# Performance work log

Measured on AMD Instinct MI355X. Metric: run time of the kernel, lower is better.

The kernel has to match this reference:

```python
import jax, jax.numpy as jnp
import numpy as np

B, T, D, H, QK, V, M = 2, 2048, 1024, 16, 64, 64, 1024
SOFTCAP = 50.0


def apply_rope(x, positions, max_wavelength=10000.0):
    # x: (B, T, H, d), positions: (T,)
    d = x.shape[-1]
    fraction = 2.0 * jnp.arange(d // 2, dtype=jnp.float32) / d
    timescale = max_wavelength ** fraction                      # (d/2,)
    sinusoid = positions.astype(jnp.float32)[:, None] / timescale  # (T, d/2)
    sin = jnp.sin(sinusoid)[:, None, :]  # (T, 1, d/2) broadcasts over heads
    cos = jnp.cos(sinusoid)[:, None, :]
    x1, x2 = jnp.split(x, 2, axis=-1)
    out = jnp.concatenate([x1 * cos - x2 * sin, x2 * cos + x1 * sin], axis=-1)
    return out.astype(x.dtype)


def rms_norm(x, scale, eps=1e-6):
    var = jnp.mean(jnp.square(x.astype(jnp.float32)), axis=-1, keepdims=True)
    normed = x * jax.lax.rsqrt(var + eps).astype(x.dtype)
    return normed * (1.0 + scale).astype(x.dtype)


def setup_inputs() -> dict:
    key = jax.random.key(0)
    ks = jax.random.split(key, 10)
    s = 0.02
    # key-padding mask: per-batch kv valid lengths (all rows have >=1536 valid keys)
    kv_lens = jnp.array([1536, 2048], dtype=jnp.int32)
    mask = (jnp.arange(T)[None, :] < kv_lens[:, None])  # (B, Tk)
    mask = jnp.broadcast_to(mask[:, None, None, :], (B, 1, T, T))
    return {
        "q": jax.random.normal(ks[0], (B, T, D), jnp.float32),
        "kv": jax.random.normal(ks[1], (B, T, D), jnp.float32),
        "mask": mask,
        "q_positions": jnp.arange(T, dtype=jnp.int32),
        "kv_positions": jnp.arange(T, dtype=jnp.int32),
        "wq": jax.random.normal(ks[2], (D, H * QK), jnp.float32) * s,
        "bq": jnp.zeros((H * QK,), jnp.float32),
        "wk": jax.random.normal(ks[3], (D, H * QK), jnp.float32) * s,
        "bk": jnp.zeros((H * QK,), jnp.float32),
        "wv": jax.random.normal(ks[4], (D, H * V), jnp.float32) * s,
        "bv": jnp.zeros((H * V,), jnp.float32),
        "q_scale": jnp.zeros((QK,), jnp.float32),
        "k_scale": jnp.zeros((QK,), jnp.float32),
        "wo": jax.random.normal(ks[5], (H * V, M), jnp.float32) * s,
        "bo": jnp.zeros((M,), jnp.float32),
    }


def reference(q, kv, mask, q_positions, kv_positions,
              wq, bq, wk, bk, wv, bv, q_scale, k_scale, wo, bo):
    qh = (q @ wq + bq).reshape(B, T, H, QK)
    kh = (kv @ wk + bk).reshape(B, T, H, QK)
    vh = (kv @ wv + bv).reshape(B, T, H, V)
    # QK RMSNorm
    qh = rms_norm(qh, q_scale)
    kh = rms_norm(kh, k_scale)
    # RoPE
    qh = apply_rope(qh, q_positions)
    kh = apply_rope(kh, kv_positions)
    # softcapped, masked attention
    logits = jnp.einsum("bthd,bThd->bhtT", qh, kh) / np.sqrt(QK).astype(jnp.float32)
    logits = SOFTCAP * jnp.tanh(logits / SOFTCAP)
    logits = jnp.where(mask, logits, -1e9)
    log_probs = jax.nn.log_softmax(logits, axis=-1)
    probs = jnp.exp(log_probs)
    probs = jnp.where(mask, probs, 0.0)
    # normalized attention entropy (B, H, T)
    entropy = -jnp.sum(probs * log_probs, axis=-1) / jnp.log(mask.sum(axis=-1))
    attn = jnp.einsum("bhtT,bThd->bthd", probs, vh).reshape(B, T, H * V)
    out = attn @ wo + bo
    return out, entropy
```

## Files before the change

### kernel.cpp

```cpp
#include <hip/hip_runtime.h>

#define BB 2
#define TT 2048
#define DD 1024
#define HH 16
#define QKD 64
#define VD 64
#define MD 1024

typedef _Float16 half4 __attribute__((ext_vector_type(4)));
typedef _Float16 half8 __attribute__((ext_vector_type(8)));
typedef __fp16 fp16x2 __attribute__((ext_vector_type(2)));
typedef float f32x4 __attribute__((ext_vector_type(4)));
typedef unsigned short us8 __attribute__((ext_vector_type(8)));
typedef unsigned short us4 __attribute__((ext_vector_type(4)));

__device__ __forceinline__ unsigned short f2h(float x){
    union { _Float16 h; unsigned short u; } c; c.h = (_Float16)x; return c.u;
}

__device__ __forceinline__ void gl16(const void* g, void* l){
    __builtin_amdgcn_global_load_lds(
        (const __attribute__((address_space(1))) void*)g,
        (__attribute__((address_space(3))) void*)l, 16, 0, 0);
}

__global__ __launch_bounds__(256) void k_prep(const float* __restrict__ q,
                                              const float* __restrict__ kv,
                                              unsigned short* __restrict__ q_bf,
                                              unsigned short* __restrict__ kv_bf,
                                              const float* __restrict__ w0,
                                              const float* __restrict__ w1,
                                              const float* __restrict__ w2,
                                              const float* __restrict__ w3,
                                              unsigned short* __restrict__ o0,
                                              unsigned short* __restrict__ o1,
                                              unsigned short* __restrict__ o2,
                                              unsigned short* __restrict__ o3,
                                              const int* __restrict__ qpos,
                                              const int* __restrict__ kpos,
                                              float* __restrict__ tabq,
                                              float* __restrict__ tabk,
                                              const unsigned char* __restrict__ mask,
                                              int* __restrict__ kvlen){
    __shared__ float smem[64*65];
    int bid = blockIdx.x, tid = threadIdx.x;
    if (bid < 8192){
        const int n = BB*TT*DD/4;
        int idx = bid*256 + tid;
        const float* src = (idx < n) ? q : kv;
        unsigned short* dst = (idx < n) ? q_bf : kv_bf;
        int i = ((idx < n) ? idx : idx - n)*4;
        const float4 v = *(const float4*)(src + i);
        us4 o; o.x = f2h(v.x); o.y = f2h(v.y); o.z = f2h(v.z); o.w = f2h(v.w);
        *(us4*)(dst + i) = o;
    } else if (bid < 9216){
        int idx2 = bid - 8192;
        int z = idx2 >> 8;
        int rc2 = idx2 & 255;
        const float* in = (z==0) ? w0 : (z==1) ? w1 : (z==2) ? w2 : w3;
        unsigned short* out = (z==0) ? o0 : (z==1) ? o1 : (z==2) ? o2 : o3;
        float (*ts)[65] = (float(*)[65])smem;
        int r0 = (rc2 & 15)*64, c0 = (rc2 >> 4)*64;
        int lr = tid >> 4, lc = (tid & 15)*4;
#pragma unroll
        for (int i = 0; i < 4; ++i){
            const float4 v = *(const float4*)(in + (long)(r0 + lr + i*16)*1024 + c0 + lc);
            ts[lr+i*16][lc+0] = v.x; ts[lr+i*16][lc+1] = v.y;
            ts[lr+i*16][lc+2] = v.z; ts[lr+i*16][lc+3] = v.w;
        }
        __syncthreads();
        int oc = tid >> 2, rc = (tid & 3)*16;
        int ocp = oc;
        if (z < 2){
            int blk = oc >> 4;
            ocp = (blk == 1) ? oc + 16 : ((blk == 2) ? oc - 16 : oc);
        }
        us8 o0v, o1v;
#pragma unroll
        for (int j = 0; j < 8; ++j){ o0v[j] = f2h(ts[rc+j][ocp]); o1v[j] = f2h(ts[rc+8+j][ocp]); }
        *(us8*)(out + (long)(c0+oc)*1024 + r0 + rc)     = o0v;
        *(us8*)(out + (long)(c0+oc)*1024 + r0 + rc + 8) = o1v;
    } else if (bid < 9728){
        int gi = (bid - 9216)*256 + tid;
        const int* pos = (gi < 65536) ? qpos : kpos;
        float* tab = (gi < 65536) ? tabq : tabk;
        int idx = gi & 65535;
        int t = idx >> 5, f = idx & 31;
        float invts = expf(-((float)f*(1.f/32.f)) * 9.210340371976184f);
        float ph = (float)pos[t]*invts;
        ((float2*)tab)[idx] = make_float2(sinf(ph), cosf(ph));
    } else {
        int* red = (int*)smem;
        int b = bid - 9728;
        bool bytemode = (mask[1] != 0);
        int cnt = 0;
        for (int j = tid; j < TT; j += 256){
            long e = (long)b*TT*TT + j;
            if (bytemode) cnt += (mask[e] != 0);
            else          cnt += (((const unsigned int*)mask)[e] != 0);
        }
        red[tid] = cnt; __syncthreads();
        for (int s = 128; s > 0; s >>= 1){ if (tid < s) red[tid] += red[tid+s]; __syncthreads(); }
        if (tid == 0) kvlen[b] = red[0];
    }
}

#define GEMM_CORE(A_, Bt_, abase, bbase)                                            \
    int srow = l >> 3;                                                              \
    int scol = ((l & 7) ^ srow)*8;                                                  \
    int swb = lg ^ (li & 7);                                                        \
    const unsigned short* ga[4]; const unsigned short* gb[2];                       \
    _Pragma("unroll")                                                               \
    for (int i = 0; i < 4; ++i) ga[i] = A_  + (long)(m0 + w*32 + i*8 + srow)*1024 + scol; \
    _Pragma("unroll")                                                               \
    for (int i = 0; i < 2; ++i) gb[i] = Bt_ + (long)(n0 + w*16 + i*8 + srow)*1024 + scol; \
    _Pragma("unroll")                                                               \
    for (int i = 0; i < 4; ++i) gl16(ga[i], abase + (w*32 + i*8)*128);              \
    _Pragma("unroll")                                                               \
    for (int i = 0; i < 2; ++i) gl16(gb[i], bbase + (w*16 + i*8)*128);              \
    __syncthreads();                                                                \
    for (int ks = 0; ks < 16; ++ks){                                                \
        int cur = ks & 1;                                                           \
        if (ks + 1 < 16){                                                           \
            char* an = abase + (cur^1)*16384;                                       \
            char* bn = bbase + (cur^1)*8192;                                        \
            _Pragma("unroll")                                                       \
            for (int i = 0; i < 4; ++i){ ga[i] += 64; gl16(ga[i], an + (w*32 + i*8)*128); } \
            _Pragma("unroll")                                                       \
            for (int i = 0; i < 2; ++i){ gb[i] += 64; gl16(gb[i], bn + (w*16 + i*8)*128); } \
        }                                                                           \
        const char* ac = abase + cur*16384;                                         \
        const char* bc = bbase + cur*8192;                                          \
        _Pragma("unroll")                                                           \
        for (int kk = 0; kk < 2; ++kk){                                             \
            int co = ((kk*4) ^ swb)*16;                                             \
            half8 af[4], bf[2];                                                     \
            _Pragma("unroll")                                                       \
            for (int mi = 0; mi < 4; ++mi) af[mi] = *(const half8*)(ac + (wm + mi*16 + li)*128 + co); \
            _Pragma("unroll")                                                       \
            for (int ni = 0; ni < 2; ++ni) bf[ni] = *(const half8*)(bc + (wn + ni*16 + li)*128 + co); \
            _Pragma("unroll")                                                       \
            for (int mi = 0; mi < 4; ++mi)                                          \
                _Pragma("unroll")                                                   \
                for (int ni = 0; ni < 2; ++ni)                                      \
                    acc[mi][ni] = __builtin_amdgcn_mfma_f32_16x16x32_f16(af[mi], bf[ni], acc[mi][ni], 0, 0, 0); \
        }                                                                           \
        __syncthreads();                                                            \
    }

__global__ __launch_bounds__(256) void k_gemm3(const unsigned short* __restrict__ q_bf,
                                               const unsigned short* __restrict__ kv_bf,
                                               const unsigned short* __restrict__ wqt,
                                               const unsigned short* __restrict__ wkt,
                                               const unsigned short* __restrict__ wvt,
                                               const float* __restrict__ bq,
                                               const float* __restrict__ bk,
                                               const float* __restrict__ bv,
                                               const float* __restrict__ qscale,
                                               const float* __restrict__ kscale,
                                               const float* __restrict__ tabq,
                                               const float* __restrict__ tabk,
                                               unsigned short* __restrict__ Qr,
                                               unsigned short* __restrict__ Kr,
                                               unsigned short* __restrict__ VTb){
    __shared__ float4 smem_[3072];
    char* abase = (char*)smem_;
    char* bbase = abase + 32768;
    int flat = blockIdx.x;
    int virt = (flat & 7)*192 + (flat >> 3);
    int z = virt >> 9;
    int rem = virt & 511;
    int m0 = (rem >> 4)*128;
    int nx = rem & 15;
    int n0 = nx*64;
    const unsigned short* A  = (z == 0) ? q_bf : kv_bf;
    const unsigned short* Bt = (z == 0) ? wqt : (z == 1) ? wkt : wvt;

    int tid = threadIdx.x, l = tid & 63, w = tid >> 6;
    int lg = l >> 4, li = l & 15;
    int wm = (w >> 1)*64, wn = (w & 1)*32;
    f32x4 zero = {0.f,0.f,0.f,0.f};
    f32x4 acc[4][2];
#pragma unroll
    for (int mi = 0; mi < 4; ++mi){ acc[mi][0] = zero; acc[mi][1] = zero; }
    GEMM_CORE(A, Bt, abase, bbase)

    int hd = nx;
    if (z < 2){
        const float* bias  = (z == 0) ? bq : bk;
        const float* scale = (z == 0) ? qscale : kscale;
        const float* tab   = (z == 0) ? tabq : tabk;
        unsigned short* out = (z == 0) ? Qr : Kr;
        float* hs = (float*)smem_;
        int d0 = (wn >> 1) + li;
        float b0 = bias[hd*64 + d0];
        float b1 = bias[hd*64 + d0 + 32];
        float ssp[4][4];
#pragma unroll
        for (int mi = 0; mi < 4; ++mi)
#pragma unroll
            for (int r = 0; r < 4; ++r){
                float x0 = acc[mi][0][r] + b0;
                float x1 = acc[mi][1][r] + b1;
                ssp[mi][r] = x0*x0 + x1*x1;
            }
#pragma unroll
        for (int m = 1; m < 16; m <<= 1)
#pragma unroll
            for (int mi = 0; mi < 4; ++mi)
#pragma unroll
                for (int r = 0; r < 4; ++r) ssp[mi][r] += __shfl_xor(ssp[mi][r], m);
        if (li == 0){
#pragma unroll
            for (int mi = 0; mi < 4; ++mi)
#pragma unroll
                for (int r = 0; r < 4; ++r)
                    hs[(wm + mi*16 + lg*4 + r)*2 + (w & 1)] = ssp[mi][r];
        }
        __syncthreads();
        float sc0 = 1.f + scale[d0];
        float sc1 = 1.f + scale[d0 + 32];
#pragma unroll
        for (int mi = 0; mi < 4; ++mi)
#pragma unroll
            for (int r = 0; r < 4; ++r){
                int row = wm + mi*16 + lg*4 + r;
                float ss = hs[row*2] + hs[row*2 + 1];
                float rstd = rsqrtf(ss*(1.f/64.f) + 1e-6f);
                float x0 = (acc[mi][0][r] + b0)*rstd*sc0;
                float x1 = (acc[mi][1][r] + b1)*rstd*sc1;
                int gm = m0 + row;
                int bb = gm >> 11, t = gm & 2047;
                float2 scv = ((const float2*)tab)[t*32 + d0];
                float o0 = x0*scv.y - x1*scv.x;
                float o1 = x1*scv.y + x0*scv.x;
                long obase = ((long)(bb*HH + hd)*TT + t)*64;
                out[obase + d0]      = f2h(o0);
                out[obase + d0 + 32] = f2h(o1);
            }
    } else {
        float* Tt = (float*)smem_;
#pragma unroll
        for (int mi = 0; mi < 4; ++mi)
#pragma unroll
            for (int ni = 0; ni < 2; ++ni){
                int col = wn + ni*16 + li;
                float bb = bv[hd*64 + col];
#pragma unroll
                for (int r = 0; r < 4; ++r)
                    Tt[col*133 + wm + mi*16 + lg*4 + r] = acc[mi][ni][r] + bb;
            }
        __syncthreads();
        int bb2 = m0 >> 11, t0 = m0 & 2047;
        int vd = tid >> 2, sg = (tid & 3)*32;
        long ob = ((long)(bb2*HH + hd)*64 + vd)*TT + t0 + sg;
#pragma unroll
        for (int c = 0; c < 4; ++c){
            us8 o;
#pragma unroll
            for (int j = 0; j < 8; ++j) o[j] = f2h(Tt[vd*133 + sg + c*8 + j]);
            *(us8*)(VTb + ob + c*8) = o;
        }
    }
}

__global__ __launch_bounds__(256) void k_gemm(const unsigned short* __restrict__ A,
                                              const unsigned short* __restrict__ Bt,
                                              const float* __restrict__ bias,
                                              float* __restrict__ C, int N){
    __shared__ float4 smem_[3072];
    char* abase = (char*)smem_;
    char* bbase = abase + 32768;
    int flat = blockIdx.x;
    int virt = (flat & 7)*64 + (flat >> 3);
    int m0 = (virt >> 4)*128, n0 = (virt & 15)*64;
    int tid = threadIdx.x, l = tid & 63, w = tid >> 6;
    int lg = l >> 4, li = l & 15;
    int wm = (w >> 1)*64, wn = (w & 1)*32;
    f32x4 zero = {0.f,0.f,0.f,0.f};
    f32x4 acc[4][2];
#pragma unroll
    for (int mi = 0; mi < 4; ++mi){ acc[mi][0] = zero; acc[mi][1] = zero; }
    GEMM_CORE(A, Bt, abase, bbase)
#pragma unroll
    for (int mi = 0; mi < 4; ++mi){
#pragma unroll
        for (int ni = 0; ni < 2; ++ni){
            int row = m0 + wm + mi*16 + lg*4;
            int col = n0 + wn + ni*16 + li;
            float bb = bias[col];
#pragma unroll
            for (int r = 0; r < 4; ++r)
                C[(long)(row + r)*N + col] = acc[mi][ni][r] + bb;
        }
    }
}

__global__ __launch_bounds__(512) void k_attn(const unsigned short* __restrict__ Qr,
                                              const unsigned short* __restrict__ Kr,
                                              const unsigned short* __restrict__ VT,
                                              const int* __restrict__ kvlen,
                                              unsigned short* __restrict__ attnb,
                                              float* __restrict__ ent){
    __shared__ unsigned short Ks[2][64][64];
    __shared__ unsigned short Vs[2][64][64];
    int tid = threadIdx.x;
    int l = tid & 63, w = tid >> 6;
    int lg = l >> 4, li = l & 15;
    int flat = blockIdx.x;
    int xcd = flat & 7;
    int idx = flat >> 3;
    int qt = idx & 15;
    int g = idx >> 4;
    int bh = xcd*2 + (g & 1) + (g >> 1)*16;
    int b = bh >> 4, h = bh & 15;
    long qk0 = (long)bh * TT * 64;
    long vt0 = (long)bh * 64 * TT;
    int kvl = kvlen[b];
    int q0 = qt*128 + w*16;

    half8 qf[2];
#pragma unroll
    for (int kk = 0; kk < 2; ++kk)
        qf[kk] = *(const half8*)(Qr + qk0 + (long)(q0 + li)*64 + kk*32 + lg*8);

    int r0s = tid >> 3;
    int kcs = (tid & 7)*8;
    int sws = (((tid & 7) ^ (r0s & 7)))*16;
    char* ksb = (char*)Ks;
    char* vsb = (char*)Vs;
    int swb = (lg >> 1) ^ (li & 7);
    int off8 = (lg & 1)*8;

    {
        us8 ka = *(const us8*)(Kr + qk0 + (long)r0s*64 + kcs);
        us8 va = *(const us8*)(VT + vt0 + (long)r0s*TT + kcs);
        *(us8*)(ksb + r0s*128 + sws) = ka;
        *(us8*)(vsb + r0s*128 + sws) = va;
    }
    __syncthreads();

    f32x4 zero = {0.f,0.f,0.f,0.f};
    f32x4 oacc[4];
#pragma unroll
    for (int jv = 0; jv < 4; ++jv) oacc[jv] = zero;
    float l_r = 0.f, s1_r = 0.f;

    const float PA = 0.18033688f;
    const float PB = -3.7570183e-7f;
    const float PC = 9.3925458e-13f;

    int nkv = (kvl + 63) >> 6;
    for (int kt = 0; kt < nkv; ++kt){
        int cur = kt & 1;
        const char* kc = ksb + cur*8192;
        const char* vc = vsb + cur*8192;
        us8 ka, va;
        bool pref = (kt + 1 < nkv);
        if (pref){
            int k0n = (kt+1)*64;
            ka = *(const us8*)(Kr + qk0 + (long)(k0n + r0s)*64 + kcs);
            va = *(const us8*)(VT + vt0 + (long)r0s*TT + k0n + kcs);
        }
        f32x4 sacc[4];
#pragma unroll
        for (int jt = 0; jt < 4; ++jt) sacc[jt] = zero;
#pragma unroll
        for (int kk = 0; kk < 2; ++kk){
            int co = ((kk*4 + lg) ^ (li & 7))*16;
#pragma unroll
            for (int jt = 0; jt < 4; ++jt){
                half8 kf = *(const half8*)(kc + (jt*16 + li)*128 + co);
                sacc[jt] = __builtin_amdgcn_mfma_f32_16x16x32_f16(kf, qf[kk], sacc[jt], 0, 0, 0);
            }
        }
        float xs2[4][4];
        bool tail = (kt*64 + 64 > kvl);
        if (tail){
#pragma unroll
            for (int jt = 0; jt < 4; ++jt){
#pragma unroll
                for (int r = 0; r < 4; ++r){
                    float u = sacc[jt][r];
                    float z2 = u*u;
                    float v = u*(PA + z2*(PB + z2*PC));
                    xs2[jt][r] = (kt*64 + jt*16 + lg*4 + r < kvl) ? v : -1e30f;
                }
            }
        } else {
#pragma unroll
            for (int jt = 0; jt < 4; ++jt){
#pragma unroll
                for (int r = 0; r < 4; ++r){
                    float u = sacc[jt][r];
                    float z2 = u*u;
                    xs2[jt][r] = u*(PA + z2*(PB + z2*PC));
                }
            }
        }
        float p[4][4];
#pragma unroll
        for (int jt = 0; jt < 4; ++jt){
#pragma unroll
            for (int r = 0; r < 4; ++r){
                float pp = exp2f(xs2[jt][r]);
                p[jt][r] = pp;
                l_r  += pp;
                s1_r += pp * xs2[jt][r];
            }
        }
        half4 pa[4];
#pragma unroll
        for (int kk = 0; kk < 4; ++kk){
            union { half4 v; fp16x2 h2[2]; } up;
            up.h2[0] = __builtin_amdgcn_cvt_pkrtz(p[kk][0], p[kk][1]);
            up.h2[1] = __builtin_amdgcn_cvt_pkrtz(p[kk][2], p[kk][3]);
            pa[kk] = up.v;
        }
#pragma unroll
        for (int kk = 0; kk < 4; ++kk){
            int co = (((kk*2) ^ swb))*16 + off8;
#pragma unroll
            for (int jv = 0; jv < 4; ++jv){
                half4 vf = *(const half4*)(vc + (jv*16 + li)*128 + co);
                oacc[jv] = __builtin_amdgcn_mfma_f32_16x16x16f16(pa[kk], vf, oacc[jv], 0, 0, 0);
            }
        }
        if (pref){
            int nb = (kt+1) & 1;
            *(us8*)(ksb + nb*8192 + r0s*128 + sws) = ka;
            *(us8*)(vsb + nb*8192 + r0s*128 + sws) = va;
        }
        __syncthreads();
    }

    l_r  += __shfl_xor(l_r, 16);  l_r  += __shfl_xor(l_r, 32);
    s1_r += __shfl_xor(s1_r, 16); s1_r += __shfl_xor(s1_r, 32);

    float invl = 1.f / l_r;
    float invr[4];
#pragma unroll
    for (int r = 0; r < 4; ++r) invr[r] = __shfl(invl, lg*4 + r);
#pragma unroll
    for (int jv = 0; jv < 4; ++jv){
#pragma unroll
        for (int r = 0; r < 4; ++r){
            int qrow = q0 + lg*4 + r;
            attnb[((long)b*TT + qrow)*1024 + h*64 + jv*16 + li] = f2h(oacc[jv][r]*invr[r]);
        }
    }
    if (l < 16){
        const float LN2 = 0.6931471805599453f;
        float lse = logf(l_r);
        float s1n = s1_r*LN2;
        ent[(long)bh*TT + q0 + li] = (lse - s1n*invl) / logf((float)kvl);
    }
}

extern "C" void kernel_launch(void* const* d_in, const int* in_sizes, int n_in,
                              void* d_out, int out_size, void* d_ws, size_t ws_size,
                              hipStream_t stream){
    (void)in_sizes; (void)n_in; (void)out_size; (void)ws_size;
    const float* q      = (const float*)d_in[0];
    const float* kv     = (const float*)d_in[1];
    const unsigned char* mask = (const unsigned char*)d_in[2];
    const int*   qpos   = (const int*)d_in[3];
    const int*   kpos   = (const int*)d_in[4];
    const float* wq     = (const float*)d_in[5];
    const float* bq     = (const float*)d_in[6];
    const float* wk     = (const float*)d_in[7];
    const float* bk     = (const float*)d_in[8];
    const float* wv     = (const float*)d_in[9];
    const float* bv     = (const float*)d_in[10];
    const float* qscale = (const float*)d_in[11];
    const float* kscale = (const float*)d_in[12];
    const float* wo     = (const float*)d_in[13];
    const float* bo     = (const float*)d_in[14];
    float* out = (float*)d_out;
    float* ent = out + (long)BB*TT*MD;

    char* ws = (char*)d_ws;
    unsigned short* wqt   = (unsigned short*)(ws);
    unsigned short* wkt   = (unsigned short*)(ws + 2097152L);
    unsigned short* wvt   = (unsigned short*)(ws + 4194304L);
    unsigned short* wot   = (unsigned short*)(ws + 6291456L);
    unsigned short* q_bf  = (unsigned short*)(ws + 8388608L);
    unsigned short* kv_bf = (unsigned short*)(ws + 16777216L);
    unsigned short* Qr    = (unsigned short*)(ws + 25165824L);
    unsigned short* Kr    = (unsigned short*)(ws + 33554432L);
    unsigned short* VTb   = (unsigned short*)(ws + 41943040L);
    unsigned short* attnb = (unsigned short*)(ws + 50331648L);
    float*          tabq  = (float*)(ws + 58720256L);
    float*          tabk  = (float*)(ws + 59244544L);
    int*            kvln  = (int*)(ws + 59768832L);

    k_prep<<<9730, 256, 0, stream>>>(q, kv, q_bf, kv_bf,
                                     wq, wk, wv, wo, wqt, wkt, wvt, wot,
                                     qpos, kpos, tabq, tabk, mask, kvln);

    k_gemm3<<<1536, 256, 0, stream>>>(q_bf, kv_bf, wqt, wkt, wvt,
                                      bq, bk, bv, qscale, kscale,
                                      tabq, tabk, Qr, Kr, VTb);

    k_attn<<<512, 512, 0, stream>>>(Qr, Kr, VTb, kvln, attnb, ent);

    k_gemm<<<512, 256, 0, stream>>>(attnb, wot, bo, out, 1024);
}
```

Before: 137.7 us.

## Software-pipeline attention loop: compute next QK^T while processing current softmax/PV

Restructures the attention inner loop so the QK^T MFMAs for tile i+1 are issued before the softmax and PV of tile i, letting matrix and vector work overlap. K is now prefetched two tiles ahead and V one tile ahead, with staggered LDS double-buffer writes. Row-sum accumulators are split into four partial registers to shorten dependency chains. This raises register pressure (two score tiles live at once) and changes the buffer-indexing scheme, which must stay consistent with the synchronisation.

```diff
diff --git a/kernel.cpp b/kernel.cpp
--- a/kernel.cpp
+++ b/kernel.cpp
@@ -297,6 +297,63 @@
     }
 }
 
+#define ATTN_SMPV(I_, SACC_)                                                        \
+    {                                                                               \
+        float xs2[4][4];                                                            \
+        bool tail = ((I_)*64 + 64 > kvl);                                           \
+        if (tail){                                                                  \
+            _Pragma("unroll")                                                       \
+            for (int jt = 0; jt < 4; ++jt){                                         \
+                _Pragma("unroll")                                                   \
+                for (int r = 0; r < 4; ++r){                                        \
+                    float u = SACC_[jt][r];                                         \
+                    float z2 = u*u;                                                 \
+                    float v = u*(PA + z2*(PB + z2*PC));                             \
+                    xs2[jt][r] = ((I_)*64 + jt*16 + lg*4 + r < kvl) ? v : -1e30f;   \
+                }                                                                   \
+            }                                                                       \
+        } else {                                                                    \
+            _Pragma("unroll")                                                       \
+            for (int jt = 0; jt < 4; ++jt){                                         \
+                _Pragma("unroll")                                                   \
+                for (int r = 0; r < 4; ++r){                                        \
+                    float u = SACC_[jt][r];                                         \
+                    float z2 = u*u;                                                 \
+                    xs2[jt][r] = u*(PA + z2*(PB + z2*PC));                          \
+                }                                                                   \
+            }                                                                       \
+        }                                                                           \
+        float p[4][4];                                                              \
+        _Pragma("unroll")                                                           \
+        for (int jt = 0; jt < 4; ++jt){                                             \
+            _Pragma("unroll")                                                       \
+            for (int r = 0; r < 4; ++r){                                            \
+                float pp = exp2f(xs2[jt][r]);                                       \
+                p[jt][r] = pp;                                                      \
+                l4[r]  += pp;                                                       \
+                s14[r] += pp * xs2[jt][r];                                          \
+            }                                                                       \
+        }                                                                           \
+        half4 pa[4];                                                                \
+        _Pragma("unroll")                                                           \
+        for (int kk = 0; kk < 4; ++kk){                                             \
+            union { half4 v; fp16x2 h2[2]; } up;                                    \
+            up.h2[0] = __builtin_amdgcn_cvt_pkrtz(p[kk][0], p[kk][1]);              \
+            up.h2[1] = __builtin_amdgcn_cvt_pkrtz(p[kk][2], p[kk][3]);              \
+            pa[kk] = up.v;                                                          \
+        }                                                                           \
+        const char* vc = vsb + ((I_) & 1)*8192;                                     \
+        _Pragma("unroll")                                                           \
+        for (int kk = 0; kk < 4; ++kk){                                             \
+            int co = (((kk*2) ^ swb))*16 + off8;                                    \
+            _Pragma("unroll")                                                       \
+            for (int jv = 0; jv < 4; ++jv){                                         \
+                half4 vf = *(const half4*)(vc + (jv*16 + li)*128 + co);             \
+                oacc[jv] = __builtin_amdgcn_mfma_f32_16x16x16f16(pa[kk], vf, oacc[jv], 0, 0, 0); \
+            }                                                                       \
+        }                                                                           \
+    }
+
 __global__ __launch_bounds__(512) void k_attn(const unsigned short* __restrict__ Qr,
                                               const unsigned short* __restrict__ Kr,
                                               const unsigned short* __restrict__ VT,
@@ -333,6 +390,19 @@
     int swb = (lg >> 1) ^ (li & 7);
     int off8 = (lg & 1)*8;
 
+    f32x4 zero = {0.f,0.f,0.f,0.f};
+    f32x4 oacc[4];
+#pragma unroll
+    for (int jv = 0; jv < 4; ++jv) oacc[jv] = zero;
+    float l4[4]  = {0.f,0.f,0.f,0.f};
+    float s14[4] = {0.f,0.f,0.f,0.f};
+
+    const float PA = 0.18033688f;
+    const float PB = -3.7570183e-7f;
+    const float PC = 9.3925458e-13f;
+
+    int nkv = (kvl + 63) >> 6;
+
     {
         us8 ka = *(const us8*)(Kr + qk0 + (long)r0s*64 + kcs);
         us8 va = *(const us8*)(VT + vt0 + (long)r0s*TT + kcs);
@@ -340,101 +410,57 @@
         *(us8*)(vsb + r0s*128 + sws) = va;
     }
     __syncthreads();
-
-    f32x4 zero = {0.f,0.f,0.f,0.f};
-    f32x4 oacc[4];
-#pragma unroll
-    for (int jv = 0; jv < 4; ++jv) oacc[jv] = zero;
-    float l_r = 0.f, s1_r = 0.f;
-
-    const float PA = 0.18033688f;
-    const float PB = -3.7570183e-7f;
-    const float PC = 9.3925458e-13f;
-
-    int nkv = (kvl + 63) >> 6;
-    for (int kt = 0; kt < nkv; ++kt){
-        int cur = kt & 1;
-        const char* kc = ksb + cur*8192;
-        const char* vc = vsb + cur*8192;
+    f32x4 scur[4];
+#pragma unroll
+    for (int jt = 0; jt < 4; ++jt) scur[jt] = zero;
+#pragma unroll
+    for (int kk = 0; kk < 2; ++kk){
+        int co = ((kk*4 + lg) ^ (li & 7))*16;
+#pragma unroll
+        for (int jt = 0; jt < 4; ++jt){
+            half8 kf = *(const half8*)(ksb + (jt*16 + li)*128 + co);
+            scur[jt] = __builtin_amdgcn_mfma_f32_16x16x32_f16(kf, qf[kk], scur[jt], 0, 0, 0);
+        }
+    }
+    {
+        us8 ka = *(const us8*)(Kr + qk0 + (long)(64 + r0s)*64 + kcs);
+        *(us8*)(ksb + 8192 + r0s*128 + sws) = ka;
+    }
+    __syncthreads();
+
+    for (int i = 0; i < nkv - 1; ++i){
+        int cur = i & 1;
         us8 ka, va;
-        bool pref = (kt + 1 < nkv);
-        if (pref){
-            int k0n = (kt+1)*64;
-            ka = *(const us8*)(Kr + qk0 + (long)(k0n + r0s)*64 + kcs);
-            va = *(const us8*)(VT + vt0 + (long)r0s*TT + k0n + kcs);
-        }
-        f32x4 sacc[4];
-#pragma unroll
-        for (int jt = 0; jt < 4; ++jt) sacc[jt] = zero;
+        bool pk = (i + 2 < nkv);
+        if (pk) ka = *(const us8*)(Kr + qk0 + (long)((i+2)*64 + r0s)*64 + kcs);
+        va = *(const us8*)(VT + vt0 + (long)r0s*TT + (i+1)*64 + kcs);
+        const char* kc = ksb + ((i+1) & 1)*8192;
+        f32x4 snext[4];
+#pragma unroll
+        for (int jt = 0; jt < 4; ++jt) snext[jt] = zero;
 #pragma unroll
         for (int kk = 0; kk < 2; ++kk){
             int co = ((kk*4 + lg) ^ (li & 7))*16;
 #pragma unroll
             for (int jt = 0; jt < 4; ++jt){
                 half8 kf = *(const half8*)(kc + (jt*16 + li)*128 + co);
-                sacc[jt] = __builtin_amdgcn_mfma_f32_16x16x32_f16(kf, qf[kk], sacc[jt], 0, 0, 0);
+                snext[jt] = __builtin_amdgcn_mfma_f32_16x16x32_f16(kf, qf[kk], snext[jt], 0, 0, 0);
             }
         }
-        float xs2[4][4];
-        bool tail = (kt*64 + 64 > kvl);
-        if (tail){
-#pragma unroll
-            for (int jt = 0; jt < 4; ++jt){
-#pragma unroll
-                for (int r = 0; r < 4; ++r){
-                    float u = sacc[jt][r];
-                    float z2 = u*u;
-                    float v = u*(PA + z2*(PB + z2*PC));
-                    xs2[jt][r] = (kt*64 + jt*16 + lg*4 + r < kvl) ? v : -1e30f;
-                }
-            }
-        } else {
-#pragma unroll
-            for (int jt = 0; jt < 4; ++jt){
-#pragma unroll
-                for (int r = 0; r < 4; ++r){
-                    float u = sacc[jt][r];
-                    float z2 = u*u;
-                    xs2[jt][r] = u*(PA + z2*(PB + z2*PC));
-                }
-            }
-        }
-        float p[4][4];
-#pragma unroll
-        for (int jt = 0; jt < 4; ++jt){
-#pragma unroll
-            for (int r = 0; r < 4; ++r){
-                float pp = exp2f(xs2[jt][r]);
-                p[jt][r] = pp;
-                l_r  += pp;
-                s1_r += pp * xs2[jt][r];
-            }
-        }
-        half4 pa[4];
-#pragma unroll
-        for (int kk = 0; kk < 4; ++kk){
-            union { half4 v; fp16x2 h2[2]; } up;
-            up.h2[0] = __builtin_amdgcn_cvt_pkrtz(p[kk][0], p[kk][1]);
-            up.h2[1] = __builtin_amdgcn_cvt_pkrtz(p[kk][2], p[kk][3]);
-            pa[kk] = up.v;
-        }
-#pragma unroll
-        for (int kk = 0; kk < 4; ++kk){
-            int co = (((kk*2) ^ swb))*16 + off8;
-#pragma unroll
-            for (int jv = 0; jv < 4; ++jv){
-                half4 vf = *(const half4*)(vc + (jv*16 + li)*128 + co);
-                oacc[jv] = __builtin_amdgcn_mfma_f32_16x16x16f16(pa[kk], vf, oacc[jv], 0, 0, 0);
-            }
-        }
-        if (pref){
-            int nb = (kt+1) & 1;
-            *(us8*)(ksb + nb*8192 + r0s*128 + sws) = ka;
-            *(us8*)(vsb + nb*8192 + r0s*128 + sws) = va;
-        }
+        ATTN_SMPV(i, scur)
+        if (pk) *(us8*)(ksb + cur*8192 + r0s*128 + sws) = ka;
+        *(us8*)(vsb + ((i+1) & 1)*8192 + r0s*128 + sws) = va;
         __syncthreads();
-    }
-
+#pragma unroll
+        for (int jt = 0; jt < 4; ++jt) scur[jt] = snext[jt];
+    }
+    {
+        int i = nkv - 1;
+        ATTN_SMPV(i, scur)
+    }
+
+    float l_r  = (l4[0] + l4[1]) + (l4[2] + l4[3]);
+    float s1_r = (s14[0] + s14[1]) + (s14[2] + s14[3]);
     l_r  += __shfl_xor(l_r, 16);  l_r  += __shfl_xor(l_r, 32);
     s1_r += __shfl_xor(s1_r, 16); s1_r += __shfl_xor(s1_r, 32);
 
```

Result: no change. 135.9 us (median of 2 runs) (-1.3%).
